# Performance work log

Hardware: AMD Instinct MI355X
Metric: run time of the kernel (lower is better)

## Reference

```python
import jax, jax.numpy as jnp
import numpy as np

N_EMBD = 1024
N_HEAD = 16
HEAD_DIM = N_EMBD // N_HEAD
D_FF = 4 * N_EMBD


def dyt(x, alpha, gamma, beta):
    # Dynamic Tanh normalizer: gamma * tanh(alpha * x) + beta
    return gamma * jnp.tanh(x * alpha) + beta


def setup_inputs() -> dict:
    key = jax.random.key(0)
    ks = jax.random.split(key, 9)
    C, F = N_EMBD, D_FF
    s = 0.02
    return {
        "x": jax.random.normal(ks[0], (2, 2048, C), dtype=jnp.float32),
        "alpha": jnp.ones((1,), jnp.float32) * 0.5,
        "gamma": jnp.ones((C,), jnp.float32),
        "beta": jnp.zeros((C,), jnp.float32),
        "w_attn": jax.random.normal(ks[1], (C, 3 * C), jnp.float32) * s,
        "b_attn": jnp.zeros((3 * C,), jnp.float32),
        "w_proj": jax.random.normal(ks[2], (C, C), jnp.float32) * s,
        "b_proj": jnp.zeros((C,), jnp.float32),
        "w_fc": jax.random.normal(ks[3], (C, F), jnp.float32) * s,
        "b_fc": jnp.zeros((F,), jnp.float32),
        "w_fc2": jax.random.normal(ks[4], (F, C), jnp.float32) * s,
        "b_fc2": jnp.zeros((C,), jnp.float32),
    }


def reference(x, alpha, gamma, beta, w_attn, b_attn, w_proj, b_proj,
              w_fc, b_fc, w_fc2, b_fc2):
    B, T, C = x.shape
    H, D = N_HEAD, HEAD_DIM

    # --- attention branch (pre-norm with DyT) ---
    h = dyt(x, alpha, gamma, beta)
    qkv = h @ w_attn + b_attn                      # [B,T,3C]
    q, k, v = jnp.split(qkv, 3, axis=-1)
    q = q.reshape(B, T, H, D).transpose(0, 2, 1, 3)  # [B,H,T,D]
    k = k.reshape(B, T, H, D).transpose(0, 2, 1, 3)
    v = v.reshape(B, T, H, D).transpose(0, 2, 1, 3)

    scores = jnp.einsum('bhqd,bhkd->bhqk', q, k) / jnp.sqrt(jnp.asarray(D, x.dtype))
    causal = jnp.tril(jnp.ones((T, T), bool))
    scores = jnp.where(causal[None, None], scores, -jnp.inf)
    attn = jax.nn.softmax(scores, axis=-1)          # [B,H,T,T]
    out = jnp.einsum('bhqk,bhkd->bhqd', attn, v)    # [B,H,T,D]
    out = out.transpose(0, 2, 1, 3).reshape(B, T, C)
    x = x + (out @ w_proj + b_proj)

    # --- MLP branch (pre-norm with same DyT params, as in source) ---
    h2 = dyt(x, alpha, gamma, beta)
    mlp = jax.nn.gelu(h2 @ w_fc + b_fc, approximate=False) @ w_fc2 + b_fc2
    return x + mlp
```

## Files before the change

### kernel.cpp

```cpp
#include <hip/hip_runtime.h>
#include <cstdint>
#include <cstddef>

typedef __bf16 bf16;
typedef __bf16 bf16x8 __attribute__((ext_vector_type(8)));
typedef __bf16 bf16x4 __attribute__((ext_vector_type(4)));
typedef float f32x4 __attribute__((ext_vector_type(4)));

#define DEVI __device__ __forceinline__

DEVI void gload_lds16(const bf16* g, bf16* l) {
    __builtin_amdgcn_global_load_lds(
        (const __attribute__((address_space(1))) void*)(const void*)g,
        (__attribute__((address_space(3))) void*)(void*)l, 16, 0, 0);
}

DEVI float fast_tanh(float y) {
    float t = __builtin_amdgcn_exp2f(2.88539008f * y);
    return 1.f - 2.f * __builtin_amdgcn_rcpf(1.f + t);
}

__global__ void conv_t_kernel(const float* __restrict__ W, bf16* __restrict__ Wt,
                              int K, int N) {
    __shared__ float tile[64][65];
    const int tid = threadIdx.x;
    const int c  = tid & 63;
    const int r4 = tid >> 6;
    const int n0 = blockIdx.x * 64;
    const int k0 = blockIdx.y * 64;
#pragma unroll
    for (int r = 0; r < 64; r += 4)
        tile[r + r4][c] = W[(size_t)(k0 + r + r4) * N + n0 + c];
    __syncthreads();
#pragma unroll
    for (int r = 0; r < 64; r += 4)
        Wt[(size_t)(n0 + r + r4) * K + k0 + c] = (bf16)tile[c][r + r4];
}

__global__ void dyt_kernel(const float* __restrict__ x, const float* __restrict__ alpha,
                           const float* __restrict__ gamma, const float* __restrict__ beta,
                           bf16* __restrict__ h, int total) {
    int i4 = (blockIdx.x * 256 + threadIdx.x) * 4;
    if (i4 >= total) return;
    float a = alpha[0];
    float4 xv = *(const float4*)&x[i4];
    int c = i4 & 1023;
    float4 g  = *(const float4*)&gamma[c];
    float4 bt = *(const float4*)&beta[c];
    bf16x4 o;
    o[0] = (bf16)(g.x * fast_tanh(xv.x * a) + bt.x);
    o[1] = (bf16)(g.y * fast_tanh(xv.y * a) + bt.y);
    o[2] = (bf16)(g.z * fast_tanh(xv.z * a) + bt.z);
    o[3] = (bf16)(g.w * fast_tanh(xv.w * a) + bt.w);
    *(bf16x4*)&h[i4] = o;
}

__global__ void reduce2_kernel(const float* __restrict__ p, const float* __restrict__ bias,
                               const float* __restrict__ resid, float* __restrict__ out,
                               int total) {
    int i4 = (blockIdx.x * 256 + threadIdx.x) * 4;
    if (i4 >= total) return;
    float4 a = *(const float4*)&p[i4];
    float4 bsec = *(const float4*)&p[(size_t)total + i4];
    float4 r = *(const float4*)&resid[i4];
    int c = i4 & 1023;
    float4 bb = *(const float4*)&bias[c];
    float4 o;
    o.x = a.x + bsec.x + r.x + bb.x;
    o.y = a.y + bsec.y + r.y + bb.y;
    o.z = a.z + bsec.z + r.z + bb.z;
    o.w = a.w + bsec.w + r.w + bb.w;
    *(float4*)&out[i4] = o;
}

__global__ void reduce2_dyt_kernel(const float* __restrict__ p, const float* __restrict__ bias,
                                   const float* __restrict__ resid,
                                   float* __restrict__ xout, bf16* __restrict__ hout,
                                   const float* __restrict__ alpha,
                                   const float* __restrict__ gamma,
                                   const float* __restrict__ beta, int total) {
    int i4 = (blockIdx.x * 256 + threadIdx.x) * 4;
    if (i4 >= total) return;
    float a = alpha[0];
    float4 p0 = *(const float4*)&p[i4];
    float4 p1 = *(const float4*)&p[(size_t)total + i4];
    float4 r  = *(const float4*)&resid[i4];
    int c = i4 & 1023;
    float4 bb = *(const float4*)&bias[c];
    float4 g  = *(const float4*)&gamma[c];
    float4 bt = *(const float4*)&beta[c];
    float4 v;
    v.x = p0.x + p1.x + r.x + bb.x;
    v.y = p0.y + p1.y + r.y + bb.y;
    v.z = p0.z + p1.z + r.z + bb.z;
    v.w = p0.w + p1.w + r.w + bb.w;
    *(float4*)&xout[i4] = v;
    bf16x4 o;
    o[0] = (bf16)(g.x * fast_tanh(v.x * a) + bt.x);
    o[1] = (bf16)(g.y * fast_tanh(v.y * a) + bt.y);
    o[2] = (bf16)(g.z * fast_tanh(v.z * a) + bt.z);
    o[3] = (bf16)(g.w * fast_tanh(v.w * a) + bt.w);
    *(bf16x4*)&hout[i4] = o;
}

template<int OP>
__global__ void gemm_kernel(const bf16* __restrict__ A, const bf16* __restrict__ Wt,
                            const float* __restrict__ bias, const float* resid,
                            float* outf, bf16* outb,
                            const float* __restrict__ alpha_p,
                            const float* __restrict__ gamma,
                            const float* __restrict__ beta,
                            int M, int N, int K, int lda, int ldb) {
    __shared__ bf16 As[2][128 * 32];
    __shared__ bf16 Bs[2][128 * 32];
    const int tid  = threadIdx.x;
    const int lane = tid & 63;
    const int w    = tid >> 6;
    const int wr   = w >> 1, wc = w & 1;

    const int nwgx = gridDim.x;
    const int nwg  = gridDim.x * gridDim.y;
    const int orig = blockIdx.y * nwgx + blockIdx.x;
    const int cpx  = nwg >> 3;
    const int swz  = (orig & 7) * cpx + (orig >> 3);
    const int bm = (swz / nwgx) * 128;
    const int bn = (swz % nwgx) * 128;
    const int kz = blockIdx.z * K;

    f32x4 acc[4][4] = {};

    const int srow = tid >> 2;
    const int sgrp = ((tid & 3) ^ ((srow >> 1) & 3)) * 8;
    const bf16* a0 = A  + (size_t)(bm + srow) * lda + kz + sgrp;
    const bf16* a1 = a0 + (size_t)64 * lda;
    const bf16* b0 = Wt + (size_t)(bn + srow) * ldb + kz + sgrp;
    const bf16* b1 = b0 + (size_t)64 * ldb;

    auto stage = [&](int buf) {
        gload_lds16(a0, &As[buf][tid * 8]);
        gload_lds16(a1, &As[buf][2048 + tid * 8]);
        gload_lds16(b0, &Bs[buf][tid * 8]);
        gload_lds16(b1, &Bs[buf][2048 + tid * 8]);
        a0 += 32; a1 += 32; b0 += 32; b1 += 32;
    };

    const int lh = lane >> 4, lm = lane & 15;
    const int arow = wr * 64 + lm;
    const int brow = wc * 64 + lm;
    const int gsw = (lh ^ ((lm >> 1) & 3)) * 8;

    stage(0);
    __syncthreads();

    const int nk = K >> 5;
    for (int kt = 0; kt < nk; ++kt) {
        const int cur = kt & 1;
        if (kt + 1 < nk) stage(cur ^ 1);
        bf16x8 af[4], bfr[4];
#pragma unroll
        for (int i = 0; i < 4; i++)
            af[i] = *(const bf16x8*)&As[cur][(arow + i * 16) * 32 + gsw];
#pragma unroll
        for (int i = 0; i < 4; i++)
            bfr[i] = *(const bf16x8*)&Bs[cur][(brow + i * 16) * 32 + gsw];
#pragma unroll
        for (int i = 0; i < 4; i++)
#pragma unroll
            for (int j = 0; j < 4; j++)
                acc[i][j] = __builtin_amdgcn_mfma_f32_16x16x32_bf16(af[i], bfr[j], acc[i][j], 0, 0, 0);
        __syncthreads();
    }

#pragma unroll
    for (int i = 0; i < 4; i++) {
        const int row0 = bm + wr * 64 + i * 16 + lh * 4;
#pragma unroll
        for (int jf = 0; jf < 4; jf++) {
            const int col = bn + wc * 64 + jf * 16 + lm;
            const float bval = (OP == 4) ? 0.f : bias[col];
#pragma unroll
            for (int r = 0; r < 4; r++) {
                const int row = row0 + r;
                const size_t idx = (size_t)row * N + col;
                float v = acc[i][jf][r] + bval;
                if (OP == 0) {
                    const float qs = (col < 1024) ? 0.18033688011f : 1.0f;
                    outb[idx] = (bf16)(v * qs);
                } else if (OP == 1) {
                    v += resid[idx];
                    outf[idx] = v;
                    float hh = gamma[col] * fast_tanh(v * alpha_p[0]) + beta[col];
                    outb[idx] = (bf16)hh;
                } else if (OP == 2) {
                    float xc = v * (1.f + 0.044715f * v * v);
                    float g = v * __builtin_amdgcn_rcpf(
                        1.f + __builtin_amdgcn_exp2f(-2.30220795f * xc));
                    outb[idx] = (bf16)g;
                } else if (OP == 3) {
                    v += resid[idx];
                    outf[idx] = v;
                } else {
                    outf[(size_t)blockIdx.z * M * N + idx] = v;
                }
            }
        }
    }
}

__global__ void attn_kernel(const bf16* __restrict__ qkv, bf16* __restrict__ out) {
    const int j  = blockIdx.x;
    const int bh = blockIdx.y;
    const int b = bh >> 4, h = bh & 15;
    const int tid = threadIdx.x, lane = tid & 63, w = tid >> 6;
    const int T = 2048;
    const size_t C3 = 3072;
    const bf16* qb = qkv + (size_t)b * T * C3 + h * 64;
    const bf16* kb = qb + 1024;
    const bf16* vb = qb + 2048;

    __shared__ bf16 Ks[2][64][64];
    __shared__ bf16 Vt[2][64][68];
    __shared__ bf16 Pl[4][16][68];

    const int tA = j, tB = 31 - j;
    const int qA = tA * 64 + w * 16;
    const int qB = tB * 64 + w * 16;
    const int lm = lane & 15;
    const int lh = lane >> 4;

    bf16x8 qfA0, qfA1, qfB0, qfB1;
    {
        size_t qo = (size_t)(qA + lm) * C3 + lh * 8;
        qfA0 = *(const bf16x8*)&qb[qo];
        qfA1 = *(const bf16x8*)&qb[qo + 32];
        qo = (size_t)(qB + lm) * C3 + lh * 8;
        qfB0 = *(const bf16x8*)&qb[qo];
        qfB1 = *(const bf16x8*)&qb[qo + 32];
    }
    f32x4 accA[4] = {}, accB[4] = {};
    float mA = -1e30f, lA = 0.f, mB = -1e30f, lB = 0.f;

    const int nt = tB + 1;
    const int sg = tid & 7;
    const int sq = tid >> 3;
    bf16x8 rv[4];

    const int krow = tid >> 3;
    const int kcb  = tid & 7;
    const int kcbs = (kcb ^ (krow & 7)) * 8;
    auto stageK = [&](int buf, int k0) {
        gload_lds16(&kb[(size_t)(k0 + krow) * C3 + kcbs],      &Ks[buf][0][0]  + tid * 8);
        gload_lds16(&kb[(size_t)(k0 + 32 + krow) * C3 + kcbs], &Ks[buf][32][0] + tid * 8);
    };
    auto loadV = [&](int k0) {
        if (tid < 128) {
#pragma unroll
            for (int i = 0; i < 4; ++i)
                rv[i] = *(const bf16x8*)&vb[(size_t)(k0 + sq * 4 + i) * C3 + sg * 8];
        }
    };
    auto writeV = [&](int buf) {
        if (tid < 128) {
            const int cbase = ((((sq >> 1) ^ sg) & 7) << 3) + ((sq & 1) << 2);
#pragma unroll
            for (int e = 0; e < 8; ++e) {
                bf16x4 wv;
                wv[0] = rv[0][e]; wv[1] = rv[1][e]; wv[2] = rv[2][e]; wv[3] = rv[3][e];
                *(bf16x4*)&Vt[buf][sg * 8 + e][cbase] = wv;
            }
        }
    };

    auto pass = [&](const bf16x8& q0, const bf16x8& q1, f32x4 (&acc)[4],
                    float& mS, float& lS, int qg, bool diag, int buf, int k0) {
        f32x4 s[4];
        __builtin_amdgcn_s_setprio(1);
#pragma unroll
        for (int f = 0; f < 4; ++f) {
            const int row = f * 16 + lm;
            const int sw = (row & 7);
            bf16x8 kf0v = *(const bf16x8*)&Ks[buf][row][(lh ^ sw) * 8];
            bf16x8 kf1v = *(const bf16x8*)&Ks[buf][row][((lh + 4) ^ sw) * 8];
            f32x4 z = {};
            z = __builtin_amdgcn_mfma_f32_16x16x32_bf16(kf0v, q0, z, 0, 0, 0);
            z = __builtin_amdgcn_mfma_f32_16x16x32_bf16(kf1v, q1, z, 0, 0, 0);
            s[f] = z;
        }
        __builtin_amdgcn_s_setprio(0);
        if (diag) {
#pragma unroll
            for (int f = 0; f < 4; ++f)
#pragma unroll
                for (int r = 0; r < 4; ++r) {
                    const int kgl = k0 + f * 16 + lh * 4 + r;
                    s[f][r] = (kgl > qg) ? -1e30f : s[f][r];
                }
        }
        float a0 = fmaxf(fmaxf(s[0][0], s[0][1]), s[0][2]);
        float a1 = fmaxf(fmaxf(s[0][3], s[1][0]), s[1][1]);
        float a2 = fmaxf(fmaxf(s[1][2], s[1][3]), s[2][0]);
        float a3 = fmaxf(fmaxf(s[2][1], s[2][2]), s[2][3]);
        float a4 = fmaxf(fmaxf(s[3][0], s[3][1]), s[3][2]);
        float b0 = fmaxf(fmaxf(a0, a1), a2);
        float b1 = fmaxf(fmaxf(a3, a4), s[3][3]);
        float pm = fmaxf(b0, b1);
        pm = fmaxf(pm, __shfl_xor(pm, 16));
        pm = fmaxf(pm, __shfl_xor(pm, 32));
        if (!__all(pm - mS <= 8.f)) {
            const float mnew = fmaxf(mS, pm);
            const float corr = __builtin_amdgcn_exp2f(mS - mnew);
            mS = mnew;
            lS *= corr;
#pragma unroll
            for (int df = 0; df < 4; ++df)
#pragma unroll
                for (int r = 0; r < 4; ++r) acc[df][r] *= corr;
        }
        float rs = 0.f;
#pragma unroll
        for (int f = 0; f < 4; ++f) {
            bf16x4 pw;
#pragma unroll
            for (int r = 0; r < 4; ++r) {
                const float pv = __builtin_amdgcn_exp2f(s[f][r] - mS);
                rs += pv;
                pw[r] = (bf16)pv;
            }
            *(bf16x4*)&Pl[w][lm][f * 16 + lh * 4] = pw;
        }
        rs += __shfl_xor(rs, 16);
        rs += __shfl_xor(rs, 32);
        lS += rs;
        __builtin_amdgcn_s_setprio(1);
#pragma unroll
        for (int kk = 0; kk < 2; ++kk) {
            bf16x8 pa = *(const bf16x8*)&Pl[w][lm][kk * 32 + lh * 8];
            const int kblk = 4 * kk + lh;
#pragma unroll
            for (int df = 0; df < 4; ++df) {
                const int dr = df * 16 + lm;
                bf16x8 vf = *(const bf16x8*)&Vt[buf][dr][((kblk ^ ((dr >> 3) & 7)) << 3)];
                acc[df] = __builtin_amdgcn_mfma_f32_16x16x32_bf16(vf, pa, acc[df], 0, 0, 0);
            }
        }
        __builtin_amdgcn_s_setprio(0);
    };

    stageK(0, 0);
    loadV(0);
    writeV(0);
    __syncthreads();

    for (int kt = 0; kt < nt; ++kt) {
        const int k0 = kt * 64;
        const int buf = kt & 1;
        if (kt + 1 < nt) {
            stageK(buf ^ 1, k0 + 64);
            loadV(k0 + 64);
        }
        if (kt <= tA)
            pass(qfA0, qfA1, accA, mA, lA, qA + lm, kt == tA, buf, k0);
        if (kt + 1 < nt) writeV(buf ^ 1);
        pass(qfB0, qfB1, accB, mB, lB, qB + lm, kt == tB, buf, k0);
        __syncthreads();
    }

    bf16* obase = out + (size_t)b * T * 1024 + h * 64;
    {
        const float linv = 1.0f / lA;
        bf16* ob = obase + (size_t)(qA + lm) * 1024;
#pragma unroll
        for (int df = 0; df < 4; ++df) {
            bf16x4 st;
#pragma unroll
            for (int r = 0; r < 4; ++r) st[r] = (bf16)(accA[df][r] * linv);
            *(bf16x4*)&ob[df * 16 + lh * 4] = st;
        }
    }
    {
        const float linv = 1.0f / lB;
        bf16* ob = obase + (size_t)(qB + lm) * 1024;
#pragma unroll
        for (int df = 0; df < 4; ++df) {
            bf16x4 st;
#pragma unroll
            for (int r = 0; r < 4; ++r) st[r] = (bf16)(accB[df][r] * linv);
            *(bf16x4*)&ob[df * 16 + lh * 4] = st;
        }
    }
}

extern "C" void kernel_launch(void* const* d_in, const int* in_sizes, int n_in,
                              void* d_out, int out_size, void* d_ws, size_t ws_size,
                              hipStream_t stream) {
    const float* x      = (const float*)d_in[0];
    const float* alpha  = (const float*)d_in[1];
    const float* gamma  = (const float*)d_in[2];
    const float* beta   = (const float*)d_in[3];
    const float* w_attn = (const float*)d_in[4];
    const float* b_attn = (const float*)d_in[5];
    const float* w_proj = (const float*)d_in[6];
    const float* b_proj = (const float*)d_in[7];
    const float* w_fc   = (const float*)d_in[8];
    const float* b_fc   = (const float*)d_in[9];
    const float* w_fc2  = (const float*)d_in[10];
    const float* b_fc2  = (const float*)d_in[11];
    float* out = (float*)d_out;

    const int M = 4096, C = 1024, F = 4096;
    char* ws = (char*)d_ws;
    bf16* wt_attn = (bf16*)ws;
    bf16* wt_proj = wt_attn + (size_t)3 * C * C;
    bf16* wt_fc   = wt_proj + (size_t)C * C;
    bf16* wt_fc2  = wt_fc   + (size_t)F * C;
    bf16* hbuf    = wt_fc2  + (size_t)C * F;
    bf16* qkvbuf  = hbuf    + (size_t)M * C;
    bf16* aout    = qkvbuf  + (size_t)M * F;
    float* x2     = (float*)(aout + (size_t)M * C);
    float* part   = x2 + (size_t)M * C;
    const size_t need = (size_t)(88 + 32) * 1024 * 1024;
    const bool splitK = ws_size >= need;

    dim3 blk(256);
    conv_t_kernel<<<dim3(3 * C / 64, C / 64), blk, 0, stream>>>(w_attn, wt_attn, C, 3 * C);
    conv_t_kernel<<<dim3(C / 64, C / 64),     blk, 0, stream>>>(w_proj, wt_proj, C, C);
    conv_t_kernel<<<dim3(F / 64, C / 64),     blk, 0, stream>>>(w_fc,   wt_fc,   C, F);
    conv_t_kernel<<<dim3(C / 64, F / 64),     blk, 0, stream>>>(w_fc2,  wt_fc2,  F, C);

    dyt_kernel<<<dim3(M * C / 1024), blk, 0, stream>>>(x, alpha, gamma, beta, hbuf, M * C);

    gemm_kernel<0><<<dim3(3 * C / 128, M / 128), blk, 0, stream>>>(
        hbuf, wt_attn, b_attn, nullptr, nullptr, qkvbuf, nullptr, nullptr, nullptr,
        M, 3 * C, C, C, C);

    attn_kernel<<<dim3(16, 32), blk, 0, stream>>>(qkvbuf, aout);

    if (splitK) {
        gemm_kernel<4><<<dim3(C / 128, M / 128, 2), blk, 0, stream>>>(
            aout, wt_proj, b_proj, nullptr, part, nullptr, nullptr, nullptr, nullptr,
            M, C, C / 2, C, C);
        reduce2_dyt_kernel<<<dim3(M * C / 1024), blk, 0, stream>>>(
            part, b_proj, x, x2, hbuf, alpha, gamma, beta, M * C);
    } else {
        gemm_kernel<1><<<dim3(C / 128, M / 128), blk, 0, stream>>>(
            aout, wt_proj, b_proj, x, x2, hbuf, alpha, gamma, beta,
            M, C, C, C, C);
    }

    gemm_kernel<2><<<dim3(F / 128, M / 128), blk, 0, stream>>>(
        hbuf, wt_fc, b_fc, nullptr, nullptr, qkvbuf, nullptr, nullptr, nullptr,
        M, F, C, C, C);

    if (splitK) {
        gemm_kernel<4><<<dim3(C / 128, M / 128, 2), blk, 0, stream>>>(
            qkvbuf, wt_fc2, b_fc2, nullptr, part, nullptr, nullptr, nullptr, nullptr,
            M, C, F / 2, F, F);
        reduce2_kernel<<<dim3(M * C / 1024), blk, 0, stream>>>(part, b_fc2, x2, out, M * C);
    } else {
        gemm_kernel<3><<<dim3(C / 128, M / 128), blk, 0, stream>>>(
            qkvbuf, wt_fc2, b_fc2, x2, out, nullptr, nullptr, nullptr, nullptr,
            M, C, F, F, F);
    }
}
```

Baseline: 247.7 us.

## Share K/V fragment loads across both query tiles in attention loop

The attention inner loop now loads the K and V fragments from LDS once per key tile and reuses them for both paired query tiles, instead of reloading them inside each pass. Both QK^T MFMA groups are issued back to back before the softmax stages, and the P buffer gets a separate slot per tile so the two softmax/PV stages do not alias. The LDS row padding changes from 68 to 72, and launch bounds of 256 threads with 2 blocks are added. The cost is higher register pressure from holding the K/V fragments and two score arrays live, which the launch bound may turn into spills.

```diff
diff --git a/kernel.cpp b/kernel.cpp
--- a/kernel.cpp
+++ b/kernel.cpp
@@ -207,7 +207,8 @@
     }
 }
 
-__global__ void attn_kernel(const bf16* __restrict__ qkv, bf16* __restrict__ out) {
+__global__ void __launch_bounds__(256, 2)
+attn_kernel(const bf16* __restrict__ qkv, bf16* __restrict__ out) {
     const int j  = blockIdx.x;
     const int bh = blockIdx.y;
     const int b = bh >> 4, h = bh & 15;
@@ -219,8 +220,8 @@
     const bf16* vb = qb + 2048;
 
     __shared__ bf16 Ks[2][64][64];
-    __shared__ bf16 Vt[2][64][68];
-    __shared__ bf16 Pl[4][16][68];
+    __shared__ bf16 Vt[2][64][72];
+    __shared__ bf16 Pl[2][4][16][72];
 
     const int tA = j, tB = 31 - j;
     const int qA = tA * 64 + w * 16;
@@ -271,22 +272,8 @@
         }
     };
 
-    auto pass = [&](const bf16x8& q0, const bf16x8& q1, f32x4 (&acc)[4],
-                    float& mS, float& lS, int qg, bool diag, int buf, int k0) {
-        f32x4 s[4];
-        __builtin_amdgcn_s_setprio(1);
-#pragma unroll
-        for (int f = 0; f < 4; ++f) {
-            const int row = f * 16 + lm;
-            const int sw = (row & 7);
-            bf16x8 kf0v = *(const bf16x8*)&Ks[buf][row][(lh ^ sw) * 8];
-            bf16x8 kf1v = *(const bf16x8*)&Ks[buf][row][((lh + 4) ^ sw) * 8];
-            f32x4 z = {};
-            z = __builtin_amdgcn_mfma_f32_16x16x32_bf16(kf0v, q0, z, 0, 0, 0);
-            z = __builtin_amdgcn_mfma_f32_16x16x32_bf16(kf1v, q1, z, 0, 0, 0);
-            s[f] = z;
-        }
-        __builtin_amdgcn_s_setprio(0);
+    auto softmax_pv = [&](f32x4 (&s)[4], f32x4 (&acc)[4], float& mS, float& lS,
+                          int qg, bool diag, int k0, int slot, bf16x8 (&vf)[2][4]) {
         if (diag) {
 #pragma unroll
             for (int f = 0; f < 4; ++f)
@@ -326,7 +313,7 @@
                 rs += pv;
                 pw[r] = (bf16)pv;
             }
-            *(bf16x4*)&Pl[w][lm][f * 16 + lh * 4] = pw;
+            *(bf16x4*)&Pl[slot][w][lm][f * 16 + lh * 4] = pw;
         }
         rs += __shfl_xor(rs, 16);
         rs += __shfl_xor(rs, 32);
@@ -334,14 +321,10 @@
         __builtin_amdgcn_s_setprio(1);
 #pragma unroll
         for (int kk = 0; kk < 2; ++kk) {
-            bf16x8 pa = *(const bf16x8*)&Pl[w][lm][kk * 32 + lh * 8];
-            const int kblk = 4 * kk + lh;
-#pragma unroll
-            for (int df = 0; df < 4; ++df) {
-                const int dr = df * 16 + lm;
-                bf16x8 vf = *(const bf16x8*)&Vt[buf][dr][((kblk ^ ((dr >> 3) & 7)) << 3)];
-                acc[df] = __builtin_amdgcn_mfma_f32_16x16x32_bf16(vf, pa, acc[df], 0, 0, 0);
-            }
+            bf16x8 pa = *(const bf16x8*)&Pl[slot][w][lm][kk * 32 + lh * 8];
+#pragma unroll
+            for (int df = 0; df < 4; ++df)
+                acc[df] = __builtin_amdgcn_mfma_f32_16x16x32_bf16(vf[kk][df], pa, acc[df], 0, 0, 0);
         }
         __builtin_amdgcn_s_setprio(0);
     };
@@ -354,14 +337,54 @@
     for (int kt = 0; kt < nt; ++kt) {
         const int k0 = kt * 64;
         const int buf = kt & 1;
-        if (kt + 1 < nt) {
+        const bool hasNext = (kt + 1 < nt);
+        if (hasNext) {
             stageK(buf ^ 1, k0 + 64);
             loadV(k0 + 64);
         }
-        if (kt <= tA)
-            pass(qfA0, qfA1, accA, mA, lA, qA + lm, kt == tA, buf, k0);
-        if (kt + 1 < nt) writeV(buf ^ 1);
-        pass(qfB0, qfB1, accB, mB, lB, qB + lm, kt == tB, buf, k0);
+
+        bf16x8 kf[4][2];
+#pragma unroll
+        for (int f = 0; f < 4; ++f) {
+            const int row = f * 16 + lm;
+            const int sw = (row & 7);
+            kf[f][0] = *(const bf16x8*)&Ks[buf][row][(lh ^ sw) * 8];
+            kf[f][1] = *(const bf16x8*)&Ks[buf][row][((lh + 4) ^ sw) * 8];
+        }
+        bf16x8 vf[2][4];
+#pragma unroll
+        for (int kk = 0; kk < 2; ++kk)
+#pragma unroll
+            for (int df = 0; df < 4; ++df) {
+                const int dr = df * 16 + lm;
+                vf[kk][df] = *(const bf16x8*)&Vt[buf][dr][(((4 * kk + lh) ^ ((dr >> 3) & 7)) << 3)];
+            }
+
+        const bool actA = (kt <= tA);
+        f32x4 sA[4], sB[4];
+        __builtin_amdgcn_s_setprio(1);
+#pragma unroll
+        for (int f = 0; f < 4; ++f) {
+            f32x4 z = {};
+            z = __builtin_amdgcn_mfma_f32_16x16x32_bf16(kf[f][0], qfB0, z, 0, 0, 0);
+            z = __builtin_amdgcn_mfma_f32_16x16x32_bf16(kf[f][1], qfB1, z, 0, 0, 0);
+            sB[f] = z;
+        }
+        if (actA) {
+#pragma unroll
+            for (int f = 0; f < 4; ++f) {
+                f32x4 z = {};
+                z = __builtin_amdgcn_mfma_f32_16x16x32_bf16(kf[f][0], qfA0, z, 0, 0, 0);
+                z = __builtin_amdgcn_mfma_f32_16x16x32_bf16(kf[f][1], qfA1, z, 0, 0, 0);
+                sA[f] = z;
+            }
+        }
+        __builtin_amdgcn_s_setprio(0);
+
+        if (actA)
+            softmax_pv(sA, accA, mA, lA, qA + lm, kt == tA, k0, 0, vf);
+        if (hasNext) writeV(buf ^ 1);
+        softmax_pv(sB, accB, mB, lB, qB + lm, kt == tB, k0, 1, vf);
         __syncthreads();
     }
 
```

Result: faster. 240.7 us (-2.8%).
